# Kernel tuning notes

Hardware: AMD Instinct MI355X
Metric: run time of the kernel (lower is better)

## Reference

```python
import jax, jax.numpy as jnp
import numpy as np

SEQ, B, D_IN, D_H = 512, 64, 512, 512


def setup_inputs() -> dict:
    key = jax.random.key(0)
    ks = jax.random.split(key, 5)
    s = 1.0 / np.sqrt(D_IN + D_H)
    inp = {
        "inputs": jax.random.normal(ks[0], (SEQ, B, D_IN), dtype=jnp.float32),
        "W_f": jax.random.normal(ks[1], (D_H, D_IN + D_H), dtype=jnp.float32) * s,
        "b_f": jnp.zeros((D_H,), jnp.float32),
        "W_i": jax.random.normal(ks[2], (D_H, D_IN + D_H), dtype=jnp.float32) * s,
        "b_i": jnp.zeros((D_H,), jnp.float32),
        "W_g": jax.random.normal(ks[3], (D_H, D_IN + D_H), dtype=jnp.float32) * s,
        "b_g": jnp.zeros((D_H,), jnp.float32),
        "W_o": jax.random.normal(ks[4], (D_H, D_IN + D_H), dtype=jnp.float32) * s,
        "b_o": jnp.zeros((D_H,), jnp.float32),
    }
    return inp


def reference(inputs, W_f, b_f, W_i, b_i, W_g, b_g, W_o, b_o):
    # inputs: [seq, batch, d_in]; states start at zeros (module default)
    B_ = inputs.shape[1]
    h0 = jnp.zeros((B_, D_H), inputs.dtype)
    c0 = jnp.zeros((B_, D_H), inputs.dtype)

    def step(carry, x_t):
        hx, cx = carry
        combined = jnp.concatenate([x_t, hx], axis=1)  # [B, d_in+d_h]
        f = jax.nn.sigmoid(combined @ W_f.T + b_f)
        i = jax.nn.sigmoid(combined @ W_i.T + b_i)
        g = jnp.tanh(combined @ W_g.T + b_g)
        o = jax.nn.sigmoid(combined @ W_o.T + b_o)
        cx = f * cx + i * g
        hx = o * jnp.tanh(cx)
        return (hx, cx), hx

    (hx, cx), stacked = jax.lax.scan(step, (h0, c0), inputs)
    return stacked, hx, cx
```

## Files before the change

### kernel.cpp

```cpp
#include <hip/hip_runtime.h>

#define SEQ   512
#define BATCH 64
#define DIN   512
#define DH    512
#define KTOT  1024
#define NWG   128
#define NTH   256
#define HBUF_BYTES 65536

#define FLAGS_BYTES 65536
#define HBASE_OFF   65536
#define XBF_OFF     (HBASE_OFF + 512 * HBUF_BYTES)
#define XBF_BYTES   ((size_t)SEQ * 4 * 16 * 1024)
#define WS_MODE1    ((size_t)HBASE_OFF + 511 * HBUF_BYTES)
#define WS_MODE2    ((size_t)XBF_OFF + XBF_BYTES)
#define FLAG_STRIDE 32

typedef __attribute__((ext_vector_type(8))) short short8;
typedef __attribute__((ext_vector_type(4))) float f32x4;

__device__ __forceinline__ float tanh_fast(float v) {
    const float e = __expf(2.0f * v);
    return 1.0f - 2.0f / (e + 1.0f);
}

__device__ __forceinline__ unsigned int f2bf(float f) {
    unsigned int u = __float_as_uint(f);
    return (u + 0x7fffu + ((u >> 16) & 1u)) >> 16;
}

__device__ __forceinline__ short8 cvt8(float4 lo, float4 hi) {
    short8 r;
    r[0] = (short)f2bf(lo.x); r[1] = (short)f2bf(lo.y);
    r[2] = (short)f2bf(lo.z); r[3] = (short)f2bf(lo.w);
    r[4] = (short)f2bf(hi.x); r[5] = (short)f2bf(hi.y);
    r[6] = (short)f2bf(hi.z); r[7] = (short)f2bf(hi.w);
    return r;
}

__device__ __forceinline__ unsigned int ld_flag(const unsigned int* p) {
    return __hip_atomic_load(p, __ATOMIC_RELAXED, __HIP_MEMORY_SCOPE_AGENT);
}
__device__ __forceinline__ void st_flag(unsigned int* p, unsigned int v) {
    __hip_atomic_store(p, v, __ATOMIC_RELAXED, __HIP_MEMORY_SCOPE_AGENT);
}
__device__ __forceinline__ unsigned long long ld_h_sc1(const unsigned long long* p) {
    return __hip_atomic_load(p, __ATOMIC_RELAXED, __HIP_MEMORY_SCOPE_AGENT);
}
__device__ __forceinline__ void st_h(unsigned long long* p, unsigned long long v) {
    __hip_atomic_store(p, v, __ATOMIC_RELAXED, __HIP_MEMORY_SCOPE_AGENT);
}

__global__ __launch_bounds__(256)
void xconv(const float* __restrict__ x, unsigned short* __restrict__ xbf)
{
    const int gid = blockIdx.x * 256 + threadIdx.x;
    const int l   = gid & 63;
    const int kt  = (gid >> 6) & 15;
    const int mtt = (gid >> 10) & 3;
    const int t   = gid >> 12;
    const float* src = x + ((size_t)t * BATCH + mtt * 16 + (l & 15)) * DIN
                         + kt * 32 + (l >> 4) * 8;
    *(short8*)(xbf + (size_t)gid * 8) =
        cvt8(*(const float4*)src, *(const float4*)(src + 4));
}

template <int MODE>
__global__ __launch_bounds__(NTH, 1)
void lstm_mfma(const float* __restrict__ x,
               const unsigned short* __restrict__ xbf,
               const float* __restrict__ Wf, const float* __restrict__ bfp,
               const float* __restrict__ Wi, const float* __restrict__ bip,
               const float* __restrict__ Wg, const float* __restrict__ bgp,
               const float* __restrict__ Wo, const float* __restrict__ bop,
               float* __restrict__ out,
               unsigned int* __restrict__ ws_u32)
{
    const int tid = threadIdx.x;
    const int l   = tid & 63;
    const int mt  = tid >> 6;
    const int wg  = blockIdx.x;
    const int j0  = wg * 4;

    const int n    = l & 15;
    const int khi  = l >> 4;
    const bool isg = ((n >> 2) == 2);

    unsigned int* const flags = ws_u32;
    char* const hbase = (char*)ws_u32 + HBASE_OFF;

    const float* Wn = (n < 8) ? ((n < 4) ? Wf : Wi) : ((n < 12) ? Wg : Wo);
    const float* wrow = Wn + (size_t)(j0 + (n & 3)) * KTOT + khi * 8;
    short8 Bfr[32];
    #pragma unroll
    for (int kt = 0; kt < 32; ++kt) {
        Bfr[kt] = cvt8(*(const float4*)(wrow + kt * 32),
                       *(const float4*)(wrow + kt * 32 + 4));
    }
    const float biasn = ((n < 8) ? ((n < 4) ? bfp : bip)
                                 : ((n < 12) ? bgp : bop))[j0 + (n & 3)];

    float cst0 = 0.f, cst1 = 0.f, cst2 = 0.f, cst3 = 0.f;

    float* const hx_out = out + (size_t)SEQ * BATCH * DH;
    float* const cx_out = hx_out + (size_t)BATCH * DH;

    const int kth         = wg >> 3;
    const int lane_f_base = ((wg & 7) >> 1) << 4;
    const int half8       = (wg & 1) * 8;

    const unsigned int* const f0p = flags + (size_t)l * FLAG_STRIDE;
    const unsigned int* const f1p = f0p + (size_t)64 * FLAG_STRIDE;
    unsigned int* const my_flag = flags + (size_t)wg * FLAG_STRIDE;

    const float*  xrow_base = x + (size_t)(mt * 16 + (l & 15)) * DIN + khi * 8;
    const short8* xbf_base  = (const short8*)xbf + (size_t)mt * 16 * 64 + l;

    for (int t = 0; t < SEQ; ++t) {
        f32x4 acc = {0.f, 0.f, 0.f, 0.f};

        if (MODE == 2) {
            const short8* xp = xbf_base + (size_t)t * 4096;
            #pragma unroll
            for (int kt = 0; kt < 16; ++kt) {
                acc = __builtin_amdgcn_mfma_f32_16x16x32_bf16(xp[kt * 64], Bfr[kt],
                                                              acc, 0, 0, 0);
            }
        } else {
            const float* xr = xrow_base + (size_t)t * BATCH * DIN;
            #pragma unroll
            for (int kt = 0; kt < 16; ++kt) {
                const short8 a = cvt8(*(const float4*)(xr + kt * 32),
                                      *(const float4*)(xr + kt * 32 + 4));
                acc = __builtin_amdgcn_mfma_f32_16x16x32_bf16(a, Bfr[kt], acc, 0, 0, 0);
            }
        }

        if (t > 0) {
            if (mt == 0) {
                const unsigned int target = (unsigned int)t;
                for (;;) {
                    const unsigned int fa = ld_flag(f0p);
                    const unsigned int fb = ld_flag(f1p);
                    if (__all(fa >= target && fb >= target)) break;
                    __builtin_amdgcn_s_sleep(1);
                }
                asm volatile("" ::: "memory");
            }
            __syncthreads();

            if (MODE == 0) {
                const unsigned long long* hp =
                    (const unsigned long long*)(hbase + ((t & 1) ^ 1) * HBUF_BYTES)
                    + ((size_t)(mt * 16) * 64 + l) * 2;
                #pragma unroll
                for (int kt = 0; kt < 16; ++kt) {
                    union { unsigned long long u[2]; short8 v; } U;
                    U.u[0] = ld_h_sc1(hp + kt * 128);
                    U.u[1] = ld_h_sc1(hp + kt * 128 + 1);
                    acc = __builtin_amdgcn_mfma_f32_16x16x32_bf16(U.v, Bfr[16 + kt],
                                                                  acc, 0, 0, 0);
                }
            } else {
                const uint4* hp = (const uint4*)(hbase + (size_t)(t - 1) * HBUF_BYTES)
                                  + ((size_t)(mt * 16) * 64 + l);
                uint4 hv[16];
                #pragma unroll
                for (int kt = 0; kt < 16; ++kt) hv[kt] = hp[kt * 64];
                #pragma unroll
                for (int kt = 0; kt < 16; ++kt) {
                    union { uint4 u; short8 v; } U; U.u = hv[kt];
                    acc = __builtin_amdgcn_mfma_f32_16x16x32_bf16(U.v, Bfr[16 + kt],
                                                                  acc, 0, 0, 0);
                }
            }
        }

        float aq0, aq1, aq2, aq3;
        {
            const float m = isg ? 2.0f : 1.0f;
            const float y0 = 1.0f / (1.0f + __expf(-m * (acc[0] + biasn)));
            const float y1 = 1.0f / (1.0f + __expf(-m * (acc[1] + biasn)));
            const float y2 = 1.0f / (1.0f + __expf(-m * (acc[2] + biasn)));
            const float y3 = 1.0f / (1.0f + __expf(-m * (acc[3] + biasn)));
            aq0 = isg ? 2.0f * y0 - 1.0f : y0;
            aq1 = isg ? 2.0f * y1 - 1.0f : y1;
            aq2 = isg ? 2.0f * y2 - 1.0f : y2;
            aq3 = isg ? 2.0f * y3 - 1.0f : y3;
        }
        const float i0 = __shfl_xor(aq0, 4), g0 = __shfl_xor(aq0, 8), o0 = __shfl_xor(aq0, 12);
        const float i1 = __shfl_xor(aq1, 4), g1 = __shfl_xor(aq1, 8), o1 = __shfl_xor(aq1, 12);
        const float i2 = __shfl_xor(aq2, 4), g2 = __shfl_xor(aq2, 8), o2 = __shfl_xor(aq2, 12);
        const float i3 = __shfl_xor(aq3, 4), g3 = __shfl_xor(aq3, 8), o3 = __shfl_xor(aq3, 12);

        const bool active = ((l >> 2) & 3) == 0;
        float v0 = 0.f, v1 = 0.f, v2 = 0.f, v3 = 0.f;
        int   bT = 0;

        if (active) {
            float hq0, hq1, hq2, hq3;
            cst0 = fmaf(aq0, cst0, i0 * g0); hq0 = o0 * tanh_fast(cst0);
            cst1 = fmaf(aq1, cst1, i1 * g1); hq1 = o1 * tanh_fast(cst1);
            cst2 = fmaf(aq2, cst2, i2 * g2); hq2 = o2 * tanh_fast(cst2);
            cst3 = fmaf(aq3, cst3, i3 * g3); hq3 = o3 * tanh_fast(cst3);

            const int src = l & 48;
            const int jc  = l & 3;
            #pragma unroll
            for (int q = 0; q < 4; ++q) {
                const float hqq = (q == 0) ? hq0 : (q == 1) ? hq1 : (q == 2) ? hq2 : hq3;
                #pragma unroll
                for (int jj = 0; jj < 4; ++jj) {
                    const float tsh = __shfl(hqq, src + jj);
                    if (jc == q) {
                        if (jj == 0) v0 = tsh; else if (jj == 1) v1 = tsh;
                        else if (jj == 2) v2 = tsh; else v3 = tsh;
                    }
                }
            }
            bT = mt * 16 + ((l >> 4) << 2) + jc;

            if (t < SEQ - 1) {
                const unsigned long long pk =
                    (unsigned long long)(f2bf(v0) | (f2bf(v1) << 16))
                    | ((unsigned long long)(f2bf(v2) | (f2bf(v3) << 16)) << 32);
                char* const wb = (MODE == 0) ? hbase + (t & 1) * HBUF_BYTES
                                             : hbase + (size_t)t * HBUF_BYTES;
                unsigned long long* hp_w = (unsigned long long*)
                    (wb + (((size_t)(mt * 16 + kth) * 64
                            + (lane_f_base | (bT & 15))) << 4) + half8);
                st_h(hp_w, pk);
            }
        }

        if (t < SEQ - 1) {
            asm volatile("s_waitcnt vmcnt(0)" ::: "memory");
            __syncthreads();
            if (tid == 0) st_flag(my_flag, (unsigned int)(t + 1));
        }

        if (active) {
            const float4 ov = make_float4(v0, v1, v2, v3);
            *(float4*)(out + ((size_t)t * BATCH + bT) * DH + j0) = ov;
            if (t == SEQ - 1) {
                *(float4*)(hx_out + (size_t)bT * DH + j0) = ov;
                const int b0 = mt * 16 + ((l >> 4) << 2);
                const int j  = j0 + (l & 3);
                cx_out[(size_t)b0 * DH + j]       = cst0;
                cx_out[(size_t)(b0 + 1) * DH + j] = cst1;
                cx_out[(size_t)(b0 + 2) * DH + j] = cst2;
                cx_out[(size_t)(b0 + 3) * DH + j] = cst3;
            }
        }
    }
}

extern "C" void kernel_launch(void* const* d_in, const int* in_sizes, int n_in,
                              void* d_out, int out_size, void* d_ws, size_t ws_size,
                              hipStream_t stream)
{
    const float* x  = (const float*)d_in[0];
    const float* Wf = (const float*)d_in[1];
    const float* bf = (const float*)d_in[2];
    const float* Wi = (const float*)d_in[3];
    const float* bi = (const float*)d_in[4];
    const float* Wg = (const float*)d_in[5];
    const float* bg = (const float*)d_in[6];
    const float* Wo = (const float*)d_in[7];
    const float* bo = (const float*)d_in[8];
    float* out = (float*)d_out;

    hipMemsetAsync(d_ws, 0, FLAGS_BYTES, stream);

    unsigned int* wsp = (unsigned int*)d_ws;
    if (ws_size >= WS_MODE2) {
        unsigned short* xbf = (unsigned short*)((char*)d_ws + XBF_OFF);
        xconv<<<SEQ * 4 * 16 * 64 / 256, 256, 0, stream>>>(x, xbf);
        lstm_mfma<2><<<NWG, NTH, 0, stream>>>(x, xbf, Wf, bf, Wi, bi,
                                              Wg, bg, Wo, bo, out, wsp);
    } else if (ws_size >= WS_MODE1) {
        lstm_mfma<1><<<NWG, NTH, 0, stream>>>(x, nullptr, Wf, bf, Wi, bi,
                                              Wg, bg, Wo, bo, out, wsp);
    } else {
        lstm_mfma<0><<<NWG, NTH, 0, stream>>>(x, nullptr, Wf, bf, Wi, bi,
                                              Wg, bg, Wo, bo, out, wsp);
    }
}
```

Before: 2.329 ms.

## Swap MFMA operands to transpose gate layout and split accumulator chain

Swaps the A/B operands of each MFMA so the output tile is transposed: gates now vary across lane groups of 16 and batch across lanes, while each lane's four accumulator values cover four hidden units. This removes the 16-shuffle transpose before the h write, allows float4 bias and cx stores, and uses xor-16/32/48 shuffles to gather the gates. It also splits the serial MFMA accumulation into two independent chains to hide MFMA latency, at the cost of one extra add per element.

```diff
diff --git a/kernel.cpp b/kernel.cpp
--- a/kernel.cpp
+++ b/kernel.cpp
@@ -85,7 +85,7 @@
 
     const int n    = l & 15;
     const int khi  = l >> 4;
-    const bool isg = ((n >> 2) == 2);
+    const bool isg = (khi == 2);
 
     unsigned int* const flags = ws_u32;
     char* const hbase = (char*)ws_u32 + HBASE_OFF;
@@ -98,8 +98,8 @@
         Bfr[kt] = cvt8(*(const float4*)(wrow + kt * 32),
                        *(const float4*)(wrow + kt * 32 + 4));
     }
-    const float biasn = ((n < 8) ? ((n < 4) ? bfp : bip)
-                                 : ((n < 12) ? bgp : bop))[j0 + (n & 3)];
+    const float* bptr = (khi == 0) ? bfp : (khi == 1) ? bip : (khi == 2) ? bgp : bop;
+    const float4 bias4 = *(const float4*)(bptr + j0);
 
     float cst0 = 0.f, cst1 = 0.f, cst2 = 0.f, cst3 = 0.f;
 
@@ -118,22 +118,28 @@
     const short8* xbf_base  = (const short8*)xbf + (size_t)mt * 16 * 64 + l;
 
     for (int t = 0; t < SEQ; ++t) {
-        f32x4 acc = {0.f, 0.f, 0.f, 0.f};
+        f32x4 acc_a = {0.f, 0.f, 0.f, 0.f};
+        f32x4 acc_b = {0.f, 0.f, 0.f, 0.f};
 
         if (MODE == 2) {
             const short8* xp = xbf_base + (size_t)t * 4096;
             #pragma unroll
-            for (int kt = 0; kt < 16; ++kt) {
-                acc = __builtin_amdgcn_mfma_f32_16x16x32_bf16(xp[kt * 64], Bfr[kt],
-                                                              acc, 0, 0, 0);
+            for (int kt = 0; kt < 16; kt += 2) {
+                acc_a = __builtin_amdgcn_mfma_f32_16x16x32_bf16(Bfr[kt], xp[kt * 64],
+                                                                acc_a, 0, 0, 0);
+                acc_b = __builtin_amdgcn_mfma_f32_16x16x32_bf16(Bfr[kt + 1], xp[(kt + 1) * 64],
+                                                                acc_b, 0, 0, 0);
             }
         } else {
             const float* xr = xrow_base + (size_t)t * BATCH * DIN;
             #pragma unroll
-            for (int kt = 0; kt < 16; ++kt) {
-                const short8 a = cvt8(*(const float4*)(xr + kt * 32),
-                                      *(const float4*)(xr + kt * 32 + 4));
-                acc = __builtin_amdgcn_mfma_f32_16x16x32_bf16(a, Bfr[kt], acc, 0, 0, 0);
+            for (int kt = 0; kt < 16; kt += 2) {
+                const short8 a0 = cvt8(*(const float4*)(xr + kt * 32),
+                                       *(const float4*)(xr + kt * 32 + 4));
+                const short8 a1 = cvt8(*(const float4*)(xr + (kt + 1) * 32),
+                                       *(const float4*)(xr + (kt + 1) * 32 + 4));
+                acc_a = __builtin_amdgcn_mfma_f32_16x16x32_bf16(Bfr[kt], a0, acc_a, 0, 0, 0);
+                acc_b = __builtin_amdgcn_mfma_f32_16x16x32_bf16(Bfr[kt + 1], a1, acc_b, 0, 0, 0);
             }
         }
 
@@ -155,12 +161,16 @@
                     (const unsigned long long*)(hbase + ((t & 1) ^ 1) * HBUF_BYTES)
                     + ((size_t)(mt * 16) * 64 + l) * 2;
                 #pragma unroll
-                for (int kt = 0; kt < 16; ++kt) {
-                    union { unsigned long long u[2]; short8 v; } U;
-                    U.u[0] = ld_h_sc1(hp + kt * 128);
-                    U.u[1] = ld_h_sc1(hp + kt * 128 + 1);
-                    acc = __builtin_amdgcn_mfma_f32_16x16x32_bf16(U.v, Bfr[16 + kt],
-                                                                  acc, 0, 0, 0);
+                for (int kt = 0; kt < 16; kt += 2) {
+                    union { unsigned long long u[2]; short8 v; } U0, U1;
+                    U0.u[0] = ld_h_sc1(hp + kt * 128);
+                    U0.u[1] = ld_h_sc1(hp + kt * 128 + 1);
+                    U1.u[0] = ld_h_sc1(hp + (kt + 1) * 128);
+                    U1.u[1] = ld_h_sc1(hp + (kt + 1) * 128 + 1);
+                    acc_a = __builtin_amdgcn_mfma_f32_16x16x32_bf16(Bfr[16 + kt], U0.v,
+                                                                    acc_a, 0, 0, 0);
+                    acc_b = __builtin_amdgcn_mfma_f32_16x16x32_bf16(Bfr[17 + kt], U1.v,
+                                                                    acc_b, 0, 0, 0);
                 }
             } else {
                 const uint4* hp = (const uint4*)(hbase + (size_t)(t - 1) * HBUF_BYTES)
@@ -169,10 +179,13 @@
                 #pragma unroll
                 for (int kt = 0; kt < 16; ++kt) hv[kt] = hp[kt * 64];
                 #pragma unroll
-                for (int kt = 0; kt < 16; ++kt) {
-                    union { uint4 u; short8 v; } U; U.u = hv[kt];
-                    acc = __builtin_amdgcn_mfma_f32_16x16x32_bf16(U.v, Bfr[16 + kt],
-                                                                  acc, 0, 0, 0);
+                for (int kt = 0; kt < 16; kt += 2) {
+                    union { uint4 u; short8 v; } U0, U1;
+                    U0.u = hv[kt]; U1.u = hv[kt + 1];
+                    acc_a = __builtin_amdgcn_mfma_f32_16x16x32_bf16(Bfr[16 + kt], U0.v,
+                                                                    acc_a, 0, 0, 0);
+                    acc_b = __builtin_amdgcn_mfma_f32_16x16x32_bf16(Bfr[17 + kt], U1.v,
+                                                                    acc_b, 0, 0, 0);
                 }
             }
         }
@@ -180,56 +193,42 @@
         float aq0, aq1, aq2, aq3;
         {
             const float m = isg ? 2.0f : 1.0f;
-            const float y0 = 1.0f / (1.0f + __expf(-m * (acc[0] + biasn)));
-            const float y1 = 1.0f / (1.0f + __expf(-m * (acc[1] + biasn)));
-            const float y2 = 1.0f / (1.0f + __expf(-m * (acc[2] + biasn)));
-            const float y3 = 1.0f / (1.0f + __expf(-m * (acc[3] + biasn)));
+            const float p0 = acc_a[0] + acc_b[0] + bias4.x;
+            const float p1 = acc_a[1] + acc_b[1] + bias4.y;
+            const float p2 = acc_a[2] + acc_b[2] + bias4.z;
+            const float p3 = acc_a[3] + acc_b[3] + bias4.w;
+            const float y0 = 1.0f / (1.0f + __expf(-m * p0));
+            const float y1 = 1.0f / (1.0f + __expf(-m * p1));
+            const float y2 = 1.0f / (1.0f + __expf(-m * p2));
+            const float y3 = 1.0f / (1.0f + __expf(-m * p3));
             aq0 = isg ? 2.0f * y0 - 1.0f : y0;
             aq1 = isg ? 2.0f * y1 - 1.0f : y1;
             aq2 = isg ? 2.0f * y2 - 1.0f : y2;
             aq3 = isg ? 2.0f * y3 - 1.0f : y3;
         }
-        const float i0 = __shfl_xor(aq0, 4), g0 = __shfl_xor(aq0, 8), o0 = __shfl_xor(aq0, 12);
-        const float i1 = __shfl_xor(aq1, 4), g1 = __shfl_xor(aq1, 8), o1 = __shfl_xor(aq1, 12);
-        const float i2 = __shfl_xor(aq2, 4), g2 = __shfl_xor(aq2, 8), o2 = __shfl_xor(aq2, 12);
-        const float i3 = __shfl_xor(aq3, 4), g3 = __shfl_xor(aq3, 8), o3 = __shfl_xor(aq3, 12);
-
-        const bool active = ((l >> 2) & 3) == 0;
-        float v0 = 0.f, v1 = 0.f, v2 = 0.f, v3 = 0.f;
-        int   bT = 0;
+        const float i0 = __shfl_xor(aq0, 16), g0 = __shfl_xor(aq0, 32), o0 = __shfl_xor(aq0, 48);
+        const float i1 = __shfl_xor(aq1, 16), g1 = __shfl_xor(aq1, 32), o1 = __shfl_xor(aq1, 48);
+        const float i2 = __shfl_xor(aq2, 16), g2 = __shfl_xor(aq2, 32), o2 = __shfl_xor(aq2, 48);
+        const float i3 = __shfl_xor(aq3, 16), g3 = __shfl_xor(aq3, 32), o3 = __shfl_xor(aq3, 48);
+
+        const bool active = (l < 16);
+        float hq0 = 0.f, hq1 = 0.f, hq2 = 0.f, hq3 = 0.f;
 
         if (active) {
-            float hq0, hq1, hq2, hq3;
             cst0 = fmaf(aq0, cst0, i0 * g0); hq0 = o0 * tanh_fast(cst0);
             cst1 = fmaf(aq1, cst1, i1 * g1); hq1 = o1 * tanh_fast(cst1);
             cst2 = fmaf(aq2, cst2, i2 * g2); hq2 = o2 * tanh_fast(cst2);
             cst3 = fmaf(aq3, cst3, i3 * g3); hq3 = o3 * tanh_fast(cst3);
 
-            const int src = l & 48;
-            const int jc  = l & 3;
-            #pragma unroll
-            for (int q = 0; q < 4; ++q) {
-                const float hqq = (q == 0) ? hq0 : (q == 1) ? hq1 : (q == 2) ? hq2 : hq3;
-                #pragma unroll
-                for (int jj = 0; jj < 4; ++jj) {
-                    const float tsh = __shfl(hqq, src + jj);
-                    if (jc == q) {
-                        if (jj == 0) v0 = tsh; else if (jj == 1) v1 = tsh;
-                        else if (jj == 2) v2 = tsh; else v3 = tsh;
-                    }
-                }
-            }
-            bT = mt * 16 + ((l >> 4) << 2) + jc;
-
             if (t < SEQ - 1) {
                 const unsigned long long pk =
-                    (unsigned long long)(f2bf(v0) | (f2bf(v1) << 16))
-                    | ((unsigned long long)(f2bf(v2) | (f2bf(v3) << 16)) << 32);
+                    (unsigned long long)(f2bf(hq0) | (f2bf(hq1) << 16))
+                    | ((unsigned long long)(f2bf(hq2) | (f2bf(hq3) << 16)) << 32);
                 char* const wb = (MODE == 0) ? hbase + (t & 1) * HBUF_BYTES
                                              : hbase + (size_t)t * HBUF_BYTES;
                 unsigned long long* hp_w = (unsigned long long*)
                     (wb + (((size_t)(mt * 16 + kth) * 64
-                            + (lane_f_base | (bT & 15))) << 4) + half8);
+                            + (lane_f_base | l)) << 4) + half8);
                 st_h(hp_w, pk);
             }
         }
@@ -241,16 +240,13 @@
         }
 
         if (active) {
-            const float4 ov = make_float4(v0, v1, v2, v3);
-            *(float4*)(out + ((size_t)t * BATCH + bT) * DH + j0) = ov;
+            const int b = mt * 16 + l;
+            const float4 ov = make_float4(hq0, hq1, hq2, hq3);
+            *(float4*)(out + ((size_t)t * BATCH + b) * DH + j0) = ov;
             if (t == SEQ - 1) {
-                *(float4*)(hx_out + (size_t)bT * DH + j0) = ov;
-                const int b0 = mt * 16 + ((l >> 4) << 2);
-                const int j  = j0 + (l & 3);
-                cx_out[(size_t)b0 * DH + j]       = cst0;
-                cx_out[(size_t)(b0 + 1) * DH + j] = cst1;
-                cx_out[(size_t)(b0 + 2) * DH + j] = cst2;
-                cx_out[(size_t)(b0 + 3) * DH + j] = cst3;
+                *(float4*)(hx_out + (size_t)b * DH + j0) = ov;
+                *(float4*)(cx_out + (size_t)b * DH + j0) =
+                    make_float4(cst0, cst1, cst2, cst3);
             }
         }
     }
```

New measurement: 2.286 ms. About the same (-1.9%).
